# Kernel optimization log

Hardware: AMD Instinct MI355X
Metric: run time of the kernel (lower is better)

The kernel has to match this reference:

```python
import jax, jax.numpy as jnp
import numpy as np

NEG_BIG = -9e15
ALPHA = 0.2  # LeakyReLU negative slope


def setup_inputs() -> dict:
    key = jax.random.key(0)
    k_h, k_adj, k_W, k_a = jax.random.split(key, 4)
    B, N, F_in, F_out = 16, 2048, 128, 64
    h = jax.random.normal(k_h, (B, N, F_in), dtype=jnp.float32)
    adj = jax.random.randint(k_adj, (B, N, N), 0, 2).astype(jnp.float32)
    mask = jnp.ones((B, N, 1), dtype=jnp.float32)
    W = jax.random.normal(k_W, (F_in, F_out), dtype=jnp.float32) * (1.0 / np.sqrt(F_in))
    a = jax.random.normal(k_a, (2 * F_out, 1), dtype=jnp.float32) * (1.0 / np.sqrt(2 * F_out))
    return {"h": h, "adj": adj, "mask": mask, "W": W, "a": a}


def reference(h, adj, mask, W, a):
    # h: [B,N,Fi], adj: [B,N,N], mask: [B,N,1], W: [Fi,Fo], a: [2Fo,1]
    F_out = W.shape[1]
    Wh = jnp.einsum("bnf,fo->bno", h, W)  # [B,N,Fo]
    # concat(Wh_i, Wh_j) @ a == (Wh @ a_src)_i + (Wh @ a_dst)_j  -- avoids O(B N^2 2Fo) tensor
    a_src = a[:F_out, 0]
    a_dst = a[F_out:, 0]
    f_i = Wh @ a_src  # [B,N]
    f_j = Wh @ a_dst  # [B,N]
    e = jax.nn.leaky_relu(f_i[:, :, None] + f_j[:, None, :], negative_slope=ALPHA)  # [B,N,N]
    node_mask = mask[..., 0]  # [B,N]
    edge_mask = (adj > 0).astype(e.dtype) * node_mask[:, None, :] * node_mask[:, :, None]
    attn_logits = jnp.where(edge_mask > 0, e, jnp.full_like(e, NEG_BIG))
    attention = jax.nn.softmax(attn_logits, axis=2)  # dropout p=0 -> identity
    h_prime = jnp.einsum("bij,bjo->bio", attention, Wh)  # [B,N,Fo]
    return jax.nn.relu(h_prime)
```

## Files before the change

### kernel.cpp

```cpp
#include <hip/hip_runtime.h>
#include <stdint.h>


#define BB   16
#define NN   2048
#define FIN  128
#define FO   64
#define LOG2E 1.4426950408889634f
#define NWORDS 1048576
#define NGFULL 87381

typedef float v4f __attribute__((ext_vector_type(4)));
typedef short v8s __attribute__((ext_vector_type(8)));
typedef int   v4i __attribute__((ext_vector_type(4)));
typedef unsigned int u32;
typedef unsigned long long u64;

__device__ __forceinline__ int pack_bf16(float e0, float e1) {
    unsigned a0 = __float_as_uint(e0) + 0x8000u;
    unsigned a1 = __float_as_uint(e1) + 0x8000u;
    return (int)__builtin_amdgcn_perm(a1, a0, 0x07060302u);
}

__device__ __forceinline__ void gload16(const void* g, void* l) {
    __builtin_amdgcn_global_load_lds(
        (const __attribute__((address_space(1))) u32*)g,
        (__attribute__((address_space(3))) u32*)l, 16, 0, 0);
}

__global__ __launch_bounds__(128) void k_pre(
    const float* __restrict__ h, const float* __restrict__ W,
    const float* __restrict__ a, const float* __restrict__ adj,
    float* __restrict__ fsl2, float* __restrict__ fdl2,
    unsigned short* __restrict__ whT, u64* __restrict__ mask)
{
    __shared__ float Wlds[FIN * FO];
    __shared__ float hs[64 * 129];

    const int bid = blockIdx.x;
    const int t   = threadIdx.x;

    if ((bid & 3) != 0) {
        const int cid = bid - (bid >> 2) - 1;
        const int wid = cid * 2 + (t >> 6);
        const int l   = t & 63;

        for (int g = wid; g < NGFULL; g += 3072) {
            const float* p = adj + (size_t)g * 768 + l;
            float f0  = __builtin_nontemporal_load(p);
            float f1  = __builtin_nontemporal_load(p + 64);
            float f2  = __builtin_nontemporal_load(p + 128);
            float f3  = __builtin_nontemporal_load(p + 192);
            float f4  = __builtin_nontemporal_load(p + 256);
            float f5  = __builtin_nontemporal_load(p + 320);
            float f6  = __builtin_nontemporal_load(p + 384);
            float f7  = __builtin_nontemporal_load(p + 448);
            float f8  = __builtin_nontemporal_load(p + 512);
            float f9  = __builtin_nontemporal_load(p + 576);
            float f10 = __builtin_nontemporal_load(p + 640);
            float f11 = __builtin_nontemporal_load(p + 704);
            u64 b0  = __ballot(f0  != 0.0f);
            u64 b1  = __ballot(f1  != 0.0f);
            u64 b2  = __ballot(f2  != 0.0f);
            u64 b3  = __ballot(f3  != 0.0f);
            u64 b4  = __ballot(f4  != 0.0f);
            u64 b5  = __ballot(f5  != 0.0f);
            u64 b6  = __ballot(f6  != 0.0f);
            u64 b7  = __ballot(f7  != 0.0f);
            u64 b8  = __ballot(f8  != 0.0f);
            u64 b9  = __ballot(f9  != 0.0f);
            u64 b10 = __ballot(f10 != 0.0f);
            u64 b11 = __ballot(f11 != 0.0f);
            if (l == 0) {
                v4i* mp = (v4i*)((char*)mask + (size_t)g * 96);
                v4i s0 = {(int)(u32)b0,  (int)(b0  >> 32), (int)(u32)b1,  (int)(b1  >> 32)};
                v4i s1 = {(int)(u32)b2,  (int)(b2  >> 32), (int)(u32)b3,  (int)(b3  >> 32)};
                v4i s2 = {(int)(u32)b4,  (int)(b4  >> 32), (int)(u32)b5,  (int)(b5  >> 32)};
                v4i s3 = {(int)(u32)b6,  (int)(b6  >> 32), (int)(u32)b7,  (int)(b7  >> 32)};
                v4i s4 = {(int)(u32)b8,  (int)(b8  >> 32), (int)(u32)b9,  (int)(b9  >> 32)};
                v4i s5 = {(int)(u32)b10, (int)(b10 >> 32), (int)(u32)b11, (int)(b11 >> 32)};
                mp[0] = s0; mp[1] = s1; mp[2] = s2;
                mp[3] = s3; mp[4] = s4; mp[5] = s5;
            }
        }
        if (cid == 0 && (t >> 6) == 0) {
            const float* p = adj + (size_t)NGFULL * 768 + l;
            u64 b0 = __ballot(__builtin_nontemporal_load(p)       != 0.0f);
            u64 b1 = __ballot(__builtin_nontemporal_load(p + 64)  != 0.0f);
            u64 b2 = __ballot(__builtin_nontemporal_load(p + 128) != 0.0f);
            u64 b3 = __ballot(__builtin_nontemporal_load(p + 192) != 0.0f);
            if (l == 0) {
                v4i* mp = (v4i*)((char*)mask + (size_t)NGFULL * 96);
                v4i s0 = {(int)(u32)b0, (int)(b0 >> 32), (int)(u32)b1, (int)(b1 >> 32)};
                v4i s1 = {(int)(u32)b2, (int)(b2 >> 32), (int)(u32)b3, (int)(b3 >> 32)};
                mp[0] = s0; mp[1] = s1;
            }
        }
        return;
    }

    const int tile = bid >> 2;
    const int b  = tile >> 5;
    const int n0 = (tile & 31) * 64;

    {
        const v4f* Wg = (const v4f*)W;
        v4f* Wl = (v4f*)Wlds;
        #pragma unroll
        for (int i = 0; i < 16; ++i) Wl[t + 128 * i] = Wg[t + 128 * i];
    }
    {
        const v4f* hg = (const v4f*)(h + ((size_t)b * NN + n0) * FIN);
        #pragma unroll
        for (int i = 0; i < 16; ++i) {
            int idx = t + 128 * i;
            v4f v = __builtin_nontemporal_load(hg + idx);
            int r = idx >> 5;
            int c = (idx & 31) * 4;
            float* d = &hs[r * 129 + c];
            d[0] = v[0]; d[1] = v[1]; d[2] = v[2]; d[3] = v[3];
        }
    }
    __syncthreads();

    const int rg = t & 15;
    const int og = t >> 4;

    float acc[4][8];
    #pragma unroll
    for (int r = 0; r < 4; ++r)
        #pragma unroll
        for (int k = 0; k < 8; ++k) acc[r][k] = 0.f;

    #pragma unroll 2
    for (int f = 0; f < FIN; ++f) {
        float hv[4];
        #pragma unroll
        for (int r = 0; r < 4; ++r) hv[r] = hs[(rg * 4 + r) * 129 + f];
        const v4f* wr = (const v4f*)&Wlds[f * FO + og * 8];
        v4f w0 = wr[0];
        v4f w1 = wr[1];
        #pragma unroll
        for (int r = 0; r < 4; ++r) {
            acc[r][0] += hv[r] * w0[0]; acc[r][1] += hv[r] * w0[1];
            acc[r][2] += hv[r] * w0[2]; acc[r][3] += hv[r] * w0[3];
            acc[r][4] += hv[r] * w1[0]; acc[r][5] += hv[r] * w1[1];
            acc[r][6] += hv[r] * w1[2]; acc[r][7] += hv[r] * w1[3];
        }
    }

    float fs[4] = {0.f, 0.f, 0.f, 0.f};
    float fd[4] = {0.f, 0.f, 0.f, 0.f};
    #pragma unroll
    for (int k = 0; k < 8; ++k) {
        float as = a[og * 8 + k];
        float ad = a[FO + og * 8 + k];
        #pragma unroll
        for (int r = 0; r < 4; ++r) {
            fs[r] += acc[r][k] * as;
            fd[r] += acc[r][k] * ad;
        }
    }
    __syncthreads();
    #pragma unroll
    for (int r = 0; r < 4; ++r) {
        hs[og * 64 + rg * 4 + r]       = fs[r];
        hs[512 + og * 64 + rg * 4 + r] = fd[r];
    }
    __syncthreads();
    if (t < 64) {
        float s = 0.f, d2 = 0.f;
        #pragma unroll
        for (int g = 0; g < 8; ++g) {
            s  += hs[g * 64 + t];
            d2 += hs[512 + g * 64 + t];
        }
        fsl2[b * NN + n0 + t] = s  * LOG2E;
        fdl2[b * NN + n0 + t] = d2 * LOG2E;
    }

    #pragma unroll
    for (int k = 0; k < 8; ++k) {
        int o = og * 8 + k;
        int2 pk;
        pk.x = pack_bf16(acc[0][k], acc[1][k]);
        pk.y = pack_bf16(acc[2][k], acc[3][k]);
        *(int2*)&whT[((size_t)b * FO + o) * NN + n0 + rg * 4] = pk;
    }
}

__global__ __launch_bounds__(256) void k_attn(
    const u64* __restrict__ mask, const float* __restrict__ fsl2,
    const float* __restrict__ fdl2, const unsigned short* __restrict__ whT,
    float* __restrict__ out)
{
    __shared__ char smem[49664];

    const int t    = threadIdx.x;
    const int lane = t & 63;
    const int wv   = t >> 6;
    const int lin  = blockIdx.x;
    const int xcd  = lin & 7;
    const int s    = lin >> 3;
    const int b    = xcd * 2 + (s >> 5);
    const int itile = s & 31;
    const int i_base = itile * 64 + wv * 16;
    const int m    = lane & 15;
    const int quad = lane >> 4;
    const int l    = lane;

    const float fil2 = fsl2[b * NN + i_base + m];
    {
        const v4f* fg = (const v4f*)(fdl2 + b * NN);
        v4f* fl = (v4f*)smem;
        fl[t]       = fg[t];
        fl[t + 256] = fg[t + 256];
    }
    {
        const u64* mg = mask + (size_t)b * 65536 + itile * 2048;
        #pragma unroll
        for (int k = 0; k < 8; ++k) {
            int g = k * 256 + t;
            *(u64*)(smem + 8192 + (g >> 5) * 264 + (g & 31) * 8) = mg[g];
        }
    }

    const unsigned short* wg = whT + (size_t)b * FO * NN
        + (size_t)(wv * 16 + (l >> 2)) * NN + ((l & 3) ^ (l >> 4)) * 8;
    char* Wr = smem + 25088;
    const int wdst = wv * 1024 + l * 16;

#define STAGE_W(cn, base_) do {                              \
        gload16(wg + (cn) * 64,      (base_) + wdst);        \
        gload16(wg + (cn) * 64 + 32, (base_) + 4096 + wdst); \
    } while (0)

    STAGE_W(0, Wr);
    STAGE_W(1, Wr + 8192);
    __syncthreads();

    const int pw0  = m * 64 + (quad ^ (m >> 2)) * 16;
    const int bitb = 8192 + (wv * 16 + m) * 264 + quad;

    v4i onesi = {0x3F803F80, 0x3F803F80, 0x3F803F80, 0x3F803F80};
    v8s onesf = __builtin_bit_cast(v8s, onesi);

    v4f acc0 = {0.f, 0.f, 0.f, 0.f};
    v4f acc1 = {0.f, 0.f, 0.f, 0.f};
    v4f acc2 = {0.f, 0.f, 0.f, 0.f};
    v4f acc3 = {0.f, 0.f, 0.f, 0.f};
    v4f accs = {0.f, 0.f, 0.f, 0.f};

    int rd = 0, wr = 16384;

    for (int c = 0; c < 32; ++c) {
        if (c < 31) asm volatile("s_waitcnt vmcnt(2)" ::: "memory");
        else        asm volatile("s_waitcnt vmcnt(0)" ::: "memory");
        __builtin_amdgcn_s_barrier();
        __builtin_amdgcn_sched_barrier(0);
        if (c < 30) STAGE_W(c + 2, Wr + wr);
        __builtin_amdgcn_sched_barrier(0);

        const char* wb = Wr + rd;

        #pragma unroll
        for (int ks = 0; ks < 2; ++ks) {
            unsigned bmb = *(const unsigned char*)(smem + bitb + c * 8 + ks * 4);
            v4f F0 = *(const v4f*)(smem + c * 256 + ks * 128 + quad * 32);
            v4f F1 = *(const v4f*)(smem + c * 256 + ks * 128 + quad * 32 + 16);

            float w[8];
            #pragma unroll
            for (int e = 0; e < 8; ++e) {
                float fv = (e < 4) ? F0[e] : F1[e - 4];
                float sc = fil2 + fv;
                float lr = fmaxf(sc, 0.2f * sc);
                float ex = __builtin_amdgcn_exp2f(lr);
                w[e] = (bmb & (1u << e)) ? ex : 0.0f;
            }
            v4i pk;
            pk.x = pack_bf16(w[0], w[1]);
            pk.y = pack_bf16(w[2], w[3]);
            pk.z = pack_bf16(w[4], w[5]);
            pk.w = pack_bf16(w[6], w[7]);
            v8s afrag = __builtin_bit_cast(v8s, pk);

            v8s b0 = *(const v8s*)(wb + ks * 4096 + pw0);
            v8s b1 = *(const v8s*)(wb + ks * 4096 + pw0 + 1024);
            v8s b2 = *(const v8s*)(wb + ks * 4096 + pw0 + 2048);
            v8s b3 = *(const v8s*)(wb + ks * 4096 + pw0 + 3072);

            acc0 = __builtin_amdgcn_mfma_f32_16x16x32_bf16(afrag, b0, acc0, 0, 0, 0);
            acc1 = __builtin_amdgcn_mfma_f32_16x16x32_bf16(afrag, b1, acc1, 0, 0, 0);
            acc2 = __builtin_amdgcn_mfma_f32_16x16x32_bf16(afrag, b2, acc2, 0, 0, 0);
            acc3 = __builtin_amdgcn_mfma_f32_16x16x32_bf16(afrag, b3, acc3, 0, 0, 0);
            accs = __builtin_amdgcn_mfma_f32_16x16x32_bf16(afrag, onesf, accs, 0, 0, 0);
        }

        rd += 8192; if (rd == 24576) rd = 0;
        wr += 8192; if (wr == 24576) wr = 0;
    }
#undef STAGE_W

    #pragma unroll
    for (int r = 0; r < 4; ++r) {
        float dl = accs[r];
        float inv = dl > 0.f ? 1.0f / dl : 0.f;
        size_t ro = ((size_t)(b * NN + i_base + quad * 4 + r)) * FO + m;
        __builtin_nontemporal_store(fmaxf(acc0[r] * inv, 0.f), out + ro);
        __builtin_nontemporal_store(fmaxf(acc1[r] * inv, 0.f), out + ro + 16);
        __builtin_nontemporal_store(fmaxf(acc2[r] * inv, 0.f), out + ro + 32);
        __builtin_nontemporal_store(fmaxf(acc3[r] * inv, 0.f), out + ro + 48);
    }
}

extern "C" void kernel_launch(void* const* d_in, const int* in_sizes, int n_in,
                              void* d_out, int out_size, void* d_ws, size_t ws_size,
                              hipStream_t stream)
{
    const float* h   = (const float*)d_in[0];
    const float* adj = (const float*)d_in[1];
    const float* W   = (const float*)d_in[3];
    const float* a   = (const float*)d_in[4];
    float* out = (float*)d_out;

    char* ws = (char*)d_ws;
    float* fsl2 = (float*)ws;
    float* fdl2 = (float*)(ws + 131072);
    unsigned short* whT = (unsigned short*)(ws + 262144);
    u64* mask = (u64*)(ws + 4456448);

    k_pre <<<dim3(2048), 128, 0, stream>>>(h, W, a, adj, fsl2, fdl2, whT, mask);
    k_attn<<<dim3(512),  256, 0, stream>>>(mask, fsl2, fdl2, whT, out);
}
```

Before: 433.4 us.

## Split adjacency bitmask conversion into its own streaming kernel with software-pipelined loads

The fused preprocessing kernel, which mixed adjacency-to-bitmask conversion with the Wh projection, is split into two kernels. The conversion kernel gives each wave a contiguous 8192-float chunk and double-buffers 16 nontemporal loads per lane to keep more memory traffic in flight, using 256-thread blocks with an occupancy hint. The projection gets its own 2D-grid kernel. This removes the interleaved block-role scheme but adds a kernel launch and gives up overlap between the two preprocessing jobs.

```diff
diff --git a/kernel.cpp b/kernel.cpp
--- a/kernel.cpp
+++ b/kernel.cpp
@@ -7,8 +7,6 @@
 #define FIN  128
 #define FO   64
 #define LOG2E 1.4426950408889634f
-#define NWORDS 1048576
-#define NGFULL 87381
 
 typedef float v4f __attribute__((ext_vector_type(4)));
 typedef short v8s __attribute__((ext_vector_type(8)));
@@ -28,80 +26,57 @@
         (__attribute__((address_space(3))) u32*)l, 16, 0, 0);
 }
 
-__global__ __launch_bounds__(128) void k_pre(
+__global__ __launch_bounds__(256, 6) void k_conv(
+    const float* __restrict__ adj, u64* __restrict__ mask)
+{
+    const int t = threadIdx.x;
+    const int l = t & 63;
+    const int w = blockIdx.x * 4 + (t >> 6);
+
+    const float* p = adj + (size_t)w * 8192 + l;
+    u64* mp = mask + (size_t)w * 128;
+
+    float fA[16], fB[16];
+    #pragma unroll
+    for (int k = 0; k < 16; ++k)
+        fA[k] = __builtin_nontemporal_load(p + k * 64);
+
+    #pragma unroll
+    for (int g = 0; g < 8; ++g) {
+        if (g < 7) {
+            #pragma unroll
+            for (int k = 0; k < 16; ++k)
+                fB[k] = __builtin_nontemporal_load(p + (g + 1) * 1024 + k * 64);
+        }
+        u64 bb[16];
+        #pragma unroll
+        for (int k = 0; k < 16; ++k) bb[k] = __ballot(fA[k] != 0.0f);
+        if (l == 0) {
+            v4i* sp = (v4i*)(mp + g * 16);
+            #pragma unroll
+            for (int s = 0; s < 8; ++s) {
+                v4i v = {(int)(u32)bb[2*s],     (int)(bb[2*s]     >> 32),
+                         (int)(u32)bb[2*s + 1], (int)(bb[2*s + 1] >> 32)};
+                sp[s] = v;
+            }
+        }
+        #pragma unroll
+        for (int k = 0; k < 16; ++k) fA[k] = fB[k];
+    }
+}
+
+__global__ __launch_bounds__(128) void k_wh(
     const float* __restrict__ h, const float* __restrict__ W,
-    const float* __restrict__ a, const float* __restrict__ adj,
+    const float* __restrict__ a,
     float* __restrict__ fsl2, float* __restrict__ fdl2,
-    unsigned short* __restrict__ whT, u64* __restrict__ mask)
+    unsigned short* __restrict__ whT)
 {
     __shared__ float Wlds[FIN * FO];
     __shared__ float hs[64 * 129];
 
-    const int bid = blockIdx.x;
-    const int t   = threadIdx.x;
-
-    if ((bid & 3) != 0) {
-        const int cid = bid - (bid >> 2) - 1;
-        const int wid = cid * 2 + (t >> 6);
-        const int l   = t & 63;
-
-        for (int g = wid; g < NGFULL; g += 3072) {
-            const float* p = adj + (size_t)g * 768 + l;
-            float f0  = __builtin_nontemporal_load(p);
-            float f1  = __builtin_nontemporal_load(p + 64);
-            float f2  = __builtin_nontemporal_load(p + 128);
-            float f3  = __builtin_nontemporal_load(p + 192);
-            float f4  = __builtin_nontemporal_load(p + 256);
-            float f5  = __builtin_nontemporal_load(p + 320);
-            float f6  = __builtin_nontemporal_load(p + 384);
-            float f7  = __builtin_nontemporal_load(p + 448);
-            float f8  = __builtin_nontemporal_load(p + 512);
-            float f9  = __builtin_nontemporal_load(p + 576);
-            float f10 = __builtin_nontemporal_load(p + 640);
-            float f11 = __builtin_nontemporal_load(p + 704);
-            u64 b0  = __ballot(f0  != 0.0f);
-            u64 b1  = __ballot(f1  != 0.0f);
-            u64 b2  = __ballot(f2  != 0.0f);
-            u64 b3  = __ballot(f3  != 0.0f);
-            u64 b4  = __ballot(f4  != 0.0f);
-            u64 b5  = __ballot(f5  != 0.0f);
-            u64 b6  = __ballot(f6  != 0.0f);
-            u64 b7  = __ballot(f7  != 0.0f);
-            u64 b8  = __ballot(f8  != 0.0f);
-            u64 b9  = __ballot(f9  != 0.0f);
-            u64 b10 = __ballot(f10 != 0.0f);
-            u64 b11 = __ballot(f11 != 0.0f);
-            if (l == 0) {
-                v4i* mp = (v4i*)((char*)mask + (size_t)g * 96);
-                v4i s0 = {(int)(u32)b0,  (int)(b0  >> 32), (int)(u32)b1,  (int)(b1  >> 32)};
-                v4i s1 = {(int)(u32)b2,  (int)(b2  >> 32), (int)(u32)b3,  (int)(b3  >> 32)};
-                v4i s2 = {(int)(u32)b4,  (int)(b4  >> 32), (int)(u32)b5,  (int)(b5  >> 32)};
-                v4i s3 = {(int)(u32)b6,  (int)(b6  >> 32), (int)(u32)b7,  (int)(b7  >> 32)};
-                v4i s4 = {(int)(u32)b8,  (int)(b8  >> 32), (int)(u32)b9,  (int)(b9  >> 32)};
-                v4i s5 = {(int)(u32)b10, (int)(b10 >> 32), (int)(u32)b11, (int)(b11 >> 32)};
-                mp[0] = s0; mp[1] = s1; mp[2] = s2;
-                mp[3] = s3; mp[4] = s4; mp[5] = s5;
-            }
-        }
-        if (cid == 0 && (t >> 6) == 0) {
-            const float* p = adj + (size_t)NGFULL * 768 + l;
-            u64 b0 = __ballot(__builtin_nontemporal_load(p)       != 0.0f);
-            u64 b1 = __ballot(__builtin_nontemporal_load(p + 64)  != 0.0f);
-            u64 b2 = __ballot(__builtin_nontemporal_load(p + 128) != 0.0f);
-            u64 b3 = __ballot(__builtin_nontemporal_load(p + 192) != 0.0f);
-            if (l == 0) {
-                v4i* mp = (v4i*)((char*)mask + (size_t)NGFULL * 96);
-                v4i s0 = {(int)(u32)b0, (int)(b0 >> 32), (int)(u32)b1, (int)(b1 >> 32)};
-                v4i s1 = {(int)(u32)b2, (int)(b2 >> 32), (int)(u32)b3, (int)(b3 >> 32)};
-                mp[0] = s0; mp[1] = s1;
-            }
-        }
-        return;
-    }
-
-    const int tile = bid >> 2;
-    const int b  = tile >> 5;
-    const int n0 = (tile & 31) * 64;
+    const int t  = threadIdx.x;
+    const int b  = blockIdx.y;
+    const int n0 = blockIdx.x * 64;
 
     {
         const v4f* Wg = (const v4f*)W;
@@ -330,6 +305,7 @@
     unsigned short* whT = (unsigned short*)(ws + 262144);
     u64* mask = (u64*)(ws + 4456448);
 
-    k_pre <<<dim3(2048), 128, 0, stream>>>(h, W, a, adj, fsl2, fdl2, whT, mask);
-    k_attn<<<dim3(512),  256, 0, stream>>>(mask, fsl2, fdl2, whT, out);
-}
+    k_conv<<<dim3(2048),        256, 0, stream>>>(adj, mask);
+    k_wh  <<<dim3(NN / 64, BB), 128, 0, stream>>>(h, W, a, fsl2, fdl2, whT);
+    k_attn<<<dim3(512),         256, 0, stream>>>(mask, fsl2, fdl2, whT, out);
+}
```

New measurement: 396.3 us. 1.09x faster.
